# Kernel optimization log

Hardware: AMD Instinct MI355X
Metric: run time of the kernel (lower is better)

## Reference

```python
import jax, jax.numpy as jnp
import numpy as np

N_HEADS = 16
PROJ_DIM = 64  # per-head dim
DIM = N_HEADS * PROJ_DIM  # 1024


def setup_inputs() -> dict:
    key = jax.random.key(0)
    k1, k2, k3, k4, k5 = jax.random.split(key, 5)
    N, L = 2, 2048
    scale = 1.0 / np.sqrt(DIM)
    return {
        "query": jax.random.normal(k1, (N, L, DIM), dtype=jnp.float32),
        "key": jax.random.normal(k2, (N, L, DIM), dtype=jnp.float32),
        "Wq": jax.random.normal(k3, (DIM, DIM), dtype=jnp.float32) * scale,
        "Wk": jax.random.normal(k4, (DIM, DIM), dtype=jnp.float32) * scale,
        "Wv": jax.random.normal(k5, (DIM, DIM), dtype=jnp.float32) * scale,
    }


def reference(query, key, Wq, Wk, Wv):
    # Causal linear-complexity attention (mask=True branch, left_first=False).
    N, Lq, _ = query.shape
    Lk = key.shape[1]
    H, Dh = N_HEADS, PROJ_DIM
    # torch Linear: x @ W.T ; reshape to (N, H, L, Dh)
    q = (query @ Wq.T).reshape(N, Lq, H, Dh).transpose(0, 2, 1, 3)
    k = (key @ Wk.T).reshape(N, Lk, H, Dh).transpose(0, 2, 1, 3)
    v = (key @ Wv.T).reshape(N, Lk, H, Dh).transpose(0, 2, 1, 3)
    q = jax.nn.softmax(q, axis=-1)
    k = jax.nn.softmax(k, axis=-1)
    # right[t] = sum_{s<=t} k_s^T v_s  : (N,H,Lk,Dh,Dh) cumulative outer products
    S = jnp.cumsum(jnp.einsum('nhti,nhtj->nhtij', k, v), axis=2)
    out = jnp.einsum('nhti,nhtij->nhtj', q, S)  # (N,H,Lq,Dh)
    return out.transpose(0, 2, 1, 3).reshape(N, Lq, H * Dh)
```

## Files before the change

### kernel.cpp

```cpp
#include <hip/hip_runtime.h>


constexpr int DIM  = 1024;
constexpr int H    = 16;
constexpr int DH   = 64;
constexpr int LSEQ = 2048;
constexpr int NB   = 2;
constexpr int MTOK = NB * LSEQ;
constexpr int CS   = 64;
constexpr int NC   = LSEQ / CS;

typedef __bf16 bf16x8 __attribute__((ext_vector_type(8)));
typedef float floatx4 __attribute__((ext_vector_type(4)));
typedef unsigned short ushort_t;

__device__ __forceinline__ ushort_t f2bf(float f) {
  unsigned int u = __float_as_uint(f);
  u += 0x7FFFu + ((u >> 16) & 1u);
  return (ushort_t)(u >> 16);
}
__device__ __forceinline__ float bf2f(ushort_t b) {
  return __uint_as_float(((unsigned int)b) << 16);
}

__device__ __forceinline__ void async16(void* lds, const void* g) {
  __builtin_amdgcn_global_load_lds(
      (const __attribute__((address_space(1))) unsigned int*)g,
      (__attribute__((address_space(3))) unsigned int*)lds, 16, 0, 0);
}

__device__ __forceinline__ bf16x8 tfrag(const unsigned int* T, int row, int uoff) {
  union { bf16x8 v; unsigned int u[4]; } r;
  const unsigned int* p = T + row * 33 + uoff;
  r.u[0] = p[0]; r.u[1] = p[1]; r.u[2] = p[2]; r.u[3] = p[3];
  return r.v;
}

__device__ __forceinline__ void transpose_tile(const ushort_t* g, unsigned int* TT, int tid) {
  const int ic = tid & 7, tp = tid >> 3;
  const ushort_t* r0 = g + (size_t)(2 * tp) * DIM + ic * 8;
  union { uint4 q; ushort_t u[8]; } a0, a1;
  a0.q = *(const uint4*)r0;
  a1.q = *(const uint4*)(r0 + DIM);
#pragma unroll
  for (int j = 0; j < 8; j++)
    TT[(8 * ic + j) * 33 + tp] = (unsigned int)a0.u[j] | ((unsigned int)a1.u[j] << 16);
}

__global__ __launch_bounds__(256) void cast_all(const float* __restrict__ q,
                                                const float* __restrict__ k,
                                                const float* __restrict__ wq,
                                                const float* __restrict__ wk,
                                                const float* __restrict__ wv,
                                                ushort_t* __restrict__ xbf,
                                                ushort_t* __restrict__ wbf) {
  const int seg = blockIdx.y;
  const float* src;
  ushort_t* dst;
  int n4;
  if (seg == 0)      { src = q;  dst = xbf;                  n4 = (4 << 20) / 4; }
  else if (seg == 1) { src = k;  dst = xbf + (4 << 20);      n4 = (4 << 20) / 4; }
  else if (seg == 2) { src = wq; dst = wbf;                  n4 = (1 << 20) / 4; }
  else if (seg == 3) { src = wk; dst = wbf + (1 << 20);      n4 = (1 << 20) / 4; }
  else               { src = wv; dst = wbf + (2 << 20);      n4 = (1 << 20) / 4; }
  for (int i = blockIdx.x * 256 + threadIdx.x; i < n4; i += gridDim.x * 256) {
    const float4 f = ((const float4*)src)[i];
    ((ushort4*)dst)[i] = make_ushort4(f2bf(f.x), f2bf(f.y), f2bf(f.z), f2bf(f.w));
  }
}

struct Stage { ushort_t As[128 * 32]; ushort_t Ws[128 * 32]; };
union SMemU { Stage st; ushort_t CsB[128 * 136]; };

__global__ __launch_bounds__(256) void gemm_fused(const ushort_t* __restrict__ xbf,
                                                  const ushort_t* __restrict__ wbf,
                                                  ushort_t* __restrict__ qp,
                                                  ushort_t* __restrict__ kp,
                                                  ushort_t* __restrict__ vp) {
  __shared__ SMemU sm;
  const int tid  = threadIdx.x;
  const int z    = blockIdx.z;
  const ushort_t* A = xbf + (z ? (size_t)(4 << 20) : 0);
  const ushort_t* W = wbf + (size_t)z * (1 << 20);
  ushort_t* C = (z == 0) ? qp : ((z == 1) ? kp : vp);
  const int bn   = blockIdx.x * 128;
  const int bm   = blockIdx.y * 128;
  const int lane = tid & 63;
  const int wid  = tid >> 6;
  const int wm   = wid >> 1, wn = wid & 1;
  const int row16 = lane & 15, quad = lane >> 4;

  floatx4 acc[4][4] = {};

  const ushort_t* gA0 = A + (size_t)(bm + (tid >> 2)) * DIM + (tid & 3) * 8;
  const ushort_t* gA1 = A + (size_t)(bm + 64 + (tid >> 2)) * DIM + (tid & 3) * 8;
  const ushort_t* gW0 = W + (size_t)(bn + (tid >> 2)) * DIM + (tid & 3) * 8;
  const ushort_t* gW1 = W + (size_t)(bn + 64 + (tid >> 2)) * DIM + (tid & 3) * 8;
  ushort_t* lA0 = sm.st.As + tid * 8;
  ushort_t* lA1 = sm.st.As + (tid + 256) * 8;
  ushort_t* lW0 = sm.st.Ws + tid * 8;
  ushort_t* lW1 = sm.st.Ws + (tid + 256) * 8;

  for (int k0 = 0; k0 < DIM; k0 += 32) {
    __syncthreads();
    async16(lA0, gA0 + k0);
    async16(lA1, gA1 + k0);
    async16(lW0, gW0 + k0);
    async16(lW1, gW1 + k0);
    __syncthreads();
    bf16x8 a[4], b[4];
#pragma unroll
    for (int mt = 0; mt < 4; mt++)
      a[mt] = *(const bf16x8*)&sm.st.As[(wm * 64 + mt * 16 + row16) * 32 + quad * 8];
#pragma unroll
    for (int nt = 0; nt < 4; nt++)
      b[nt] = *(const bf16x8*)&sm.st.Ws[(wn * 64 + nt * 16 + row16) * 32 + quad * 8];
#pragma unroll
    for (int mt = 0; mt < 4; mt++)
#pragma unroll
      for (int nt = 0; nt < 4; nt++)
        acc[mt][nt] = __builtin_amdgcn_mfma_f32_16x16x32_bf16(a[mt], b[nt], acc[mt][nt], 0, 0, 0);
  }
  __syncthreads();

  if (z < 2) {
#pragma unroll
    for (int mt = 0; mt < 4; mt++)
#pragma unroll
      for (int r = 0; r < 4; r++) {
        float m = fmaxf(fmaxf(acc[mt][0][r], acc[mt][1][r]),
                        fmaxf(acc[mt][2][r], acc[mt][3][r]));
#pragma unroll
        for (int o = 1; o < 16; o <<= 1) m = fmaxf(m, __shfl_xor(m, o, 64));
        float e[4], s = 0.f;
#pragma unroll
        for (int nt = 0; nt < 4; nt++) { e[nt] = __expf(acc[mt][nt][r] - m); s += e[nt]; }
#pragma unroll
        for (int o = 1; o < 16; o <<= 1) s += __shfl_xor(s, o, 64);
        const float inv = 1.f / s;
#pragma unroll
        for (int nt = 0; nt < 4; nt++) acc[mt][nt][r] = e[nt] * inv;
      }
  }

#pragma unroll
  for (int mt = 0; mt < 4; mt++)
#pragma unroll
    for (int nt = 0; nt < 4; nt++)
#pragma unroll
      for (int r = 0; r < 4; r++)
        sm.CsB[(wm * 64 + mt * 16 + quad * 4 + r) * 136 + wn * 64 + nt * 16 + row16] =
            f2bf(acc[mt][nt][r]);
  __syncthreads();
#pragma unroll
  for (int it = 0; it < 8; it++) {
    const int ch = tid + it * 256;
    const int row = ch >> 4, ic = ch & 15;
    const uint4 val = *(const uint4*)&sm.CsB[row * 136 + ic * 8];
    *(uint4*)&C[(size_t)(bm + row) * DIM + bn + ic * 8] = val;
  }
}

__global__ __launch_bounds__(256) void chunk_T(const ushort_t* __restrict__ kp,
                                               const ushort_t* __restrict__ vp,
                                               float* __restrict__ cs) {
  __shared__ unsigned int KT[64 * 33];
  __shared__ unsigned int VT[64 * 33];
  const int c = blockIdx.x, h = blockIdx.y, n = blockIdx.z;
  const int tid = threadIdx.x;
  const size_t gbase = ((size_t)(n * LSEQ + c * CS)) * DIM + h * DH;

  transpose_tile(kp + gbase, KT, tid);
  transpose_tile(vp + gbase, VT, tid);
  __syncthreads();

  const int lane = tid & 63, wid = tid >> 6;
  const int row16 = lane & 15, quad = lane >> 4;

  floatx4 acc[4] = {};
#pragma unroll
  for (int ks = 0; ks < 2; ks++) {
    const bf16x8 a = tfrag(VT, wid * 16 + row16, ks * 16 + quad * 4);
#pragma unroll
    for (int nt = 0; nt < 4; nt++) {
      const bf16x8 b = tfrag(KT, nt * 16 + row16, ks * 16 + quad * 4);
      acc[nt] = __builtin_amdgcn_mfma_f32_16x16x32_bf16(a, b, acc[nt], 0, 0, 0);
    }
  }
  float* outp = cs + ((size_t)((n * H + h) * NC + c)) * (DH * DH);
#pragma unroll
  for (int nt = 0; nt < 4; nt++)
#pragma unroll
    for (int r = 0; r < 4; r++)
      outp[(wid * 16 + quad * 4 + r) * DH + nt * 16 + row16] = acc[nt][r];
}

__global__ __launch_bounds__(256) void prefix_chunks(const float* __restrict__ cs,
                                                     ushort_t* __restrict__ csb) {
  const int nh = blockIdx.x >> 4;
  const int e  = (blockIdx.x & 15) * 256 + threadIdx.x;
  const float* bf_ = cs + (size_t)nh * NC * (DH * DH) + e;
  ushort_t* bb = csb + (size_t)nh * NC * (DH * DH) + e;
  float run = 0.f;
#pragma unroll
  for (int c = 0; c < NC; c++) {
    const float cur = bf_[(size_t)c * (DH * DH)];
    bb[(size_t)c * (DH * DH)] = f2bf(run);
    run += cur;
  }
}

__global__ __launch_bounds__(256) void attn_mfma(const ushort_t* __restrict__ qp,
                                                 const ushort_t* __restrict__ kp,
                                                 const ushort_t* __restrict__ vp,
                                                 const ushort_t* __restrict__ csb,
                                                 float* __restrict__ out) {
  __shared__ ushort_t Qs[64 * 72];
  __shared__ ushort_t Ks[64 * 72];
  __shared__ ushort_t Ts[64 * 72];
  __shared__ unsigned int VT[64 * 33];
  __shared__ ushort_t Pb[64 * 72];
  const int c = blockIdx.x, h = blockIdx.y, n = blockIdx.z;
  const int tid = threadIdx.x;
  const size_t gbase = ((size_t)(n * LSEQ + c * CS)) * DIM + h * DH;
  const size_t cbase = ((size_t)((n * H + h) * NC + c)) * (DH * DH);

#pragma unroll
  for (int it = 0; it < 2; it++) {
    const int ch = tid + it * 256;
    const int row = ch >> 3, ic = ch & 7;
    *(uint4*)&Qs[row * 72 + ic * 8] = *(const uint4*)&qp[gbase + (size_t)row * DIM + ic * 8];
    *(uint4*)&Ks[row * 72 + ic * 8] = *(const uint4*)&kp[gbase + (size_t)row * DIM + ic * 8];
    *(uint4*)&Ts[row * 72 + ic * 8] = *(const uint4*)&csb[cbase + (size_t)row * DH + ic * 8];
  }
  transpose_tile(vp + gbase, VT, tid);
  __syncthreads();

  const int lane = tid & 63, wid = tid >> 6;
  const int row16 = lane & 15, quad = lane >> 4;
  const int t0 = wid * 16;

  floatx4 acc[4] = {};
  floatx4 pacc[4] = {};

#pragma unroll
  for (int ks = 0; ks < 2; ks++) {
    const bf16x8 aq = *(const bf16x8*)&Qs[(t0 + row16) * 72 + ks * 32 + quad * 8];
#pragma unroll
    for (int nt = 0; nt < 4; nt++) {
      const bf16x8 bt = *(const bf16x8*)&Ts[(nt * 16 + row16) * 72 + ks * 32 + quad * 8];
      acc[nt] = __builtin_amdgcn_mfma_f32_16x16x32_bf16(aq, bt, acc[nt], 0, 0, 0);
      const bf16x8 bk = *(const bf16x8*)&Ks[(nt * 16 + row16) * 72 + ks * 32 + quad * 8];
      pacc[nt] = __builtin_amdgcn_mfma_f32_16x16x32_bf16(aq, bk, pacc[nt], 0, 0, 0);
    }
  }
#pragma unroll
  for (int nt = 0; nt < 4; nt++)
#pragma unroll
    for (int r = 0; r < 4; r++) {
      const int t = t0 + quad * 4 + r, s = nt * 16 + row16;
      Pb[t * 72 + s] = f2bf((s <= t) ? pacc[nt][r] : 0.f);
    }
  __syncthreads();

#pragma unroll
  for (int ks = 0; ks < 2; ks++) {
    const bf16x8 ap = *(const bf16x8*)&Pb[(t0 + row16) * 72 + ks * 32 + quad * 8];
#pragma unroll
    for (int nt = 0; nt < 4; nt++) {
      const bf16x8 bv = tfrag(VT, nt * 16 + row16, ks * 16 + quad * 4);
      acc[nt] = __builtin_amdgcn_mfma_f32_16x16x32_bf16(ap, bv, acc[nt], 0, 0, 0);
    }
  }

#pragma unroll
  for (int nt = 0; nt < 4; nt++)
#pragma unroll
    for (int r = 0; r < 4; r++)
      out[gbase + (size_t)(t0 + quad * 4 + r) * DIM + nt * 16 + row16] = acc[nt][r];
}

extern "C" void kernel_launch(void* const* d_in, const int* in_sizes, int n_in,
                              void* d_out, int out_size, void* d_ws, size_t ws_size,
                              hipStream_t stream) {
  const float* query = (const float*)d_in[0];
  const float* key   = (const float*)d_in[1];
  const float* Wq    = (const float*)d_in[2];
  const float* Wk    = (const float*)d_in[3];
  const float* Wv    = (const float*)d_in[4];
  float* out = (float*)d_out;

  const size_t PM = (size_t)4 << 20;
  ushort_t* qp = (ushort_t*)d_ws;
  ushort_t* kp = qp + PM;
  ushort_t* vp = kp + PM;
  float*    cs = (float*)(vp + PM);
  ushort_t* csb = (ushort_t*)(cs + PM);
  ushort_t* xbf = (ushort_t*)cs;
  ushort_t* wbf = (ushort_t*)out;

  cast_all<<<dim3(512, 5), 256, 0, stream>>>(query, key, Wq, Wk, Wv, xbf, wbf);

  gemm_fused<<<dim3(DIM / 128, MTOK / 128, 3), 256, 0, stream>>>(xbf, wbf, qp, kp, vp);

  chunk_T<<<dim3(NC, H, NB), 256, 0, stream>>>(kp, vp, cs);
  prefix_chunks<<<dim3(NB * H * 16), 256, 0, stream>>>(cs, csb);
  attn_mfma<<<dim3(NC, H, NB), 256, 0, stream>>>(qp, kp, vp, csb, out);
}
```

Baseline: 172.5 us.

## Fuse chunk state and prefix scan, widen GEMM K-step with swizzled LDS

Merges the per-chunk K^T V kernel and the fp32 prefix-sum kernel into one sequential scan kernel per (batch, head). It keeps the running state in registers and writes bf16 exclusive prefixes directly, removing the fp32 intermediate buffer and one launch. The GEMM now loads 64-wide K slices per barrier pair using an XOR-swizzled LDS layout to cut bank conflicts, and uses a flattened 1D grid. The attention kernel reuses the Ts buffer for P to save LDS. The scan runs on only 32 blocks serially over 32 chunks, which risks low parallelism.

```diff
diff --git a/kernel.cpp b/kernel.cpp
--- a/kernel.cpp
+++ b/kernel.cpp
@@ -22,20 +22,17 @@
 __device__ __forceinline__ float bf2f(ushort_t b) {
   return __uint_as_float(((unsigned int)b) << 16);
 }
-
 __device__ __forceinline__ void async16(void* lds, const void* g) {
   __builtin_amdgcn_global_load_lds(
       (const __attribute__((address_space(1))) unsigned int*)g,
       (__attribute__((address_space(3))) unsigned int*)lds, 16, 0, 0);
 }
-
 __device__ __forceinline__ bf16x8 tfrag(const unsigned int* T, int row, int uoff) {
   union { bf16x8 v; unsigned int u[4]; } r;
   const unsigned int* p = T + row * 33 + uoff;
   r.u[0] = p[0]; r.u[1] = p[1]; r.u[2] = p[2]; r.u[3] = p[3];
   return r.v;
 }
-
 __device__ __forceinline__ void transpose_tile(const ushort_t* g, unsigned int* TT, int tid) {
   const int ic = tid & 7, tp = tid >> 3;
   const ushort_t* r0 = g + (size_t)(2 * tp) * DIM + ic * 8;
@@ -69,88 +66,98 @@
   }
 }
 
-struct Stage { ushort_t As[128 * 32]; ushort_t Ws[128 * 32]; };
-union SMemU { Stage st; ushort_t CsB[128 * 136]; };
+union GSm {
+  struct { ushort_t A0[128 * 32]; ushort_t A1[128 * 32];
+           ushort_t W0[128 * 32]; ushort_t W1[128 * 32]; } g;
+  ushort_t CsB[128 * 136];
+};
 
 __global__ __launch_bounds__(256) void gemm_fused(const ushort_t* __restrict__ xbf,
                                                   const ushort_t* __restrict__ wbf,
                                                   ushort_t* __restrict__ qp,
                                                   ushort_t* __restrict__ kp,
                                                   ushort_t* __restrict__ vp) {
-  __shared__ SMemU sm;
-  const int tid  = threadIdx.x;
-  const int z    = blockIdx.z;
+  __shared__ GSm sm;
+  const int tid = threadIdx.x;
+  const int z   = blockIdx.x >> 8;
+  const int r   = blockIdx.x & 255;
+  const int bn  = (r & 7) * 128;
+  const int bm  = (r >> 3) * 128;
   const ushort_t* A = xbf + (z ? (size_t)(4 << 20) : 0);
   const ushort_t* W = wbf + (size_t)z * (1 << 20);
   ushort_t* C = (z == 0) ? qp : ((z == 1) ? kp : vp);
-  const int bn   = blockIdx.x * 128;
-  const int bm   = blockIdx.y * 128;
-  const int lane = tid & 63;
-  const int wid  = tid >> 6;
-  const int wm   = wid >> 1, wn = wid & 1;
+  const int lane = tid & 63, wid = tid >> 6;
+  const int wm = wid >> 1, wn = wid & 1;
   const int row16 = lane & 15, quad = lane >> 4;
 
+  const int row0 = tid >> 2, c0 = tid & 3;
+  const int cg = c0 ^ ((row0 >> 1) & 3);
+  const ushort_t* gA  = A + (size_t)(bm + row0) * DIM + cg * 8;
+  const ushort_t* gA2 = gA + (size_t)64 * DIM;
+  const ushort_t* gW  = W + (size_t)(bn + row0) * DIM + cg * 8;
+  const ushort_t* gW2 = gW + (size_t)64 * DIM;
+
   floatx4 acc[4][4] = {};
-
-  const ushort_t* gA0 = A + (size_t)(bm + (tid >> 2)) * DIM + (tid & 3) * 8;
-  const ushort_t* gA1 = A + (size_t)(bm + 64 + (tid >> 2)) * DIM + (tid & 3) * 8;
-  const ushort_t* gW0 = W + (size_t)(bn + (tid >> 2)) * DIM + (tid & 3) * 8;
-  const ushort_t* gW1 = W + (size_t)(bn + 64 + (tid >> 2)) * DIM + (tid & 3) * 8;
-  ushort_t* lA0 = sm.st.As + tid * 8;
-  ushort_t* lA1 = sm.st.As + (tid + 256) * 8;
-  ushort_t* lW0 = sm.st.Ws + tid * 8;
-  ushort_t* lW1 = sm.st.Ws + (tid + 256) * 8;
-
-  for (int k0 = 0; k0 < DIM; k0 += 32) {
-    __syncthreads();
-    async16(lA0, gA0 + k0);
-    async16(lA1, gA1 + k0);
-    async16(lW0, gW0 + k0);
-    async16(lW1, gW1 + k0);
-    __syncthreads();
-    bf16x8 a[4], b[4];
+  const int cq = quad ^ ((row16 >> 1) & 3);
+
+  for (int k0 = 0; k0 < DIM; k0 += 64) {
+    __syncthreads();
+    async16(sm.g.A0 + tid * 8, gA + k0);
+    async16(sm.g.A0 + (tid + 256) * 8, gA2 + k0);
+    async16(sm.g.A1 + tid * 8, gA + k0 + 32);
+    async16(sm.g.A1 + (tid + 256) * 8, gA2 + k0 + 32);
+    async16(sm.g.W0 + tid * 8, gW + k0);
+    async16(sm.g.W0 + (tid + 256) * 8, gW2 + k0);
+    async16(sm.g.W1 + tid * 8, gW + k0 + 32);
+    async16(sm.g.W1 + (tid + 256) * 8, gW2 + k0 + 32);
+    __syncthreads();
+#pragma unroll
+    for (int ks = 0; ks < 2; ks++) {
+      const ushort_t* As = ks ? sm.g.A1 : sm.g.A0;
+      const ushort_t* Ws = ks ? sm.g.W1 : sm.g.W0;
+      bf16x8 a[4], b[4];
+#pragma unroll
+      for (int mt = 0; mt < 4; mt++)
+        a[mt] = *(const bf16x8*)&As[(wm * 64 + mt * 16 + row16) * 32 + cq * 8];
+#pragma unroll
+      for (int nt = 0; nt < 4; nt++)
+        b[nt] = *(const bf16x8*)&Ws[(wn * 64 + nt * 16 + row16) * 32 + cq * 8];
+#pragma unroll
+      for (int mt = 0; mt < 4; mt++)
+#pragma unroll
+        for (int nt = 0; nt < 4; nt++)
+          acc[mt][nt] = __builtin_amdgcn_mfma_f32_16x16x32_bf16(a[mt], b[nt], acc[mt][nt], 0, 0, 0);
+    }
+  }
+  __syncthreads();
+
+  if (z < 2) {
 #pragma unroll
     for (int mt = 0; mt < 4; mt++)
-      a[mt] = *(const bf16x8*)&sm.st.As[(wm * 64 + mt * 16 + row16) * 32 + quad * 8];
-#pragma unroll
-    for (int nt = 0; nt < 4; nt++)
-      b[nt] = *(const bf16x8*)&sm.st.Ws[(wn * 64 + nt * 16 + row16) * 32 + quad * 8];
-#pragma unroll
-    for (int mt = 0; mt < 4; mt++)
-#pragma unroll
-      for (int nt = 0; nt < 4; nt++)
-        acc[mt][nt] = __builtin_amdgcn_mfma_f32_16x16x32_bf16(a[mt], b[nt], acc[mt][nt], 0, 0, 0);
-  }
-  __syncthreads();
-
-  if (z < 2) {
-#pragma unroll
-    for (int mt = 0; mt < 4; mt++)
-#pragma unroll
-      for (int r = 0; r < 4; r++) {
-        float m = fmaxf(fmaxf(acc[mt][0][r], acc[mt][1][r]),
-                        fmaxf(acc[mt][2][r], acc[mt][3][r]));
+#pragma unroll
+      for (int rr = 0; rr < 4; rr++) {
+        float m = fmaxf(fmaxf(acc[mt][0][rr], acc[mt][1][rr]),
+                        fmaxf(acc[mt][2][rr], acc[mt][3][rr]));
 #pragma unroll
         for (int o = 1; o < 16; o <<= 1) m = fmaxf(m, __shfl_xor(m, o, 64));
         float e[4], s = 0.f;
 #pragma unroll
-        for (int nt = 0; nt < 4; nt++) { e[nt] = __expf(acc[mt][nt][r] - m); s += e[nt]; }
+        for (int nt = 0; nt < 4; nt++) { e[nt] = __expf(acc[mt][nt][rr] - m); s += e[nt]; }
 #pragma unroll
         for (int o = 1; o < 16; o <<= 1) s += __shfl_xor(s, o, 64);
         const float inv = 1.f / s;
 #pragma unroll
-        for (int nt = 0; nt < 4; nt++) acc[mt][nt][r] = e[nt] * inv;
+        for (int nt = 0; nt < 4; nt++) acc[mt][nt][rr] = e[nt] * inv;
       }
   }
-
 #pragma unroll
   for (int mt = 0; mt < 4; mt++)
 #pragma unroll
     for (int nt = 0; nt < 4; nt++)
 #pragma unroll
-      for (int r = 0; r < 4; r++)
-        sm.CsB[(wm * 64 + mt * 16 + quad * 4 + r) * 136 + wn * 64 + nt * 16 + row16] =
-            f2bf(acc[mt][nt][r]);
+      for (int rr = 0; rr < 4; rr++)
+        sm.CsB[(wm * 64 + mt * 16 + quad * 4 + rr) * 136 + wn * 64 + nt * 16 + row16] =
+            f2bf(acc[mt][nt][rr]);
   __syncthreads();
 #pragma unroll
   for (int it = 0; it < 8; it++) {
@@ -161,52 +168,43 @@
   }
 }
 
-__global__ __launch_bounds__(256) void chunk_T(const ushort_t* __restrict__ kp,
-                                               const ushort_t* __restrict__ vp,
-                                               float* __restrict__ cs) {
+__global__ __launch_bounds__(256) void chunk_scan(const ushort_t* __restrict__ kp,
+                                                  const ushort_t* __restrict__ vp,
+                                                  ushort_t* __restrict__ Tpre) {
   __shared__ unsigned int KT[64 * 33];
   __shared__ unsigned int VT[64 * 33];
-  const int c = blockIdx.x, h = blockIdx.y, n = blockIdx.z;
+  const int h = blockIdx.x & 15, n = blockIdx.x >> 4;
   const int tid = threadIdx.x;
-  const size_t gbase = ((size_t)(n * LSEQ + c * CS)) * DIM + h * DH;
-
-  transpose_tile(kp + gbase, KT, tid);
-  transpose_tile(vp + gbase, VT, tid);
-  __syncthreads();
-
   const int lane = tid & 63, wid = tid >> 6;
   const int row16 = lane & 15, quad = lane >> 4;
 
-  floatx4 acc[4] = {};
-#pragma unroll
-  for (int ks = 0; ks < 2; ks++) {
-    const bf16x8 a = tfrag(VT, wid * 16 + row16, ks * 16 + quad * 4);
-#pragma unroll
-    for (int nt = 0; nt < 4; nt++) {
-      const bf16x8 b = tfrag(KT, nt * 16 + row16, ks * 16 + quad * 4);
-      acc[nt] = __builtin_amdgcn_mfma_f32_16x16x32_bf16(a, b, acc[nt], 0, 0, 0);
-    }
-  }
-  float* outp = cs + ((size_t)((n * H + h) * NC + c)) * (DH * DH);
-#pragma unroll
-  for (int nt = 0; nt < 4; nt++)
-#pragma unroll
-    for (int r = 0; r < 4; r++)
-      outp[(wid * 16 + quad * 4 + r) * DH + nt * 16 + row16] = acc[nt][r];
-}
-
-__global__ __launch_bounds__(256) void prefix_chunks(const float* __restrict__ cs,
-                                                     ushort_t* __restrict__ csb) {
-  const int nh = blockIdx.x >> 4;
-  const int e  = (blockIdx.x & 15) * 256 + threadIdx.x;
-  const float* bf_ = cs + (size_t)nh * NC * (DH * DH) + e;
-  ushort_t* bb = csb + (size_t)nh * NC * (DH * DH) + e;
-  float run = 0.f;
-#pragma unroll
+  floatx4 run[4] = {};
   for (int c = 0; c < NC; c++) {
-    const float cur = bf_[(size_t)c * (DH * DH)];
-    bb[(size_t)c * (DH * DH)] = f2bf(run);
-    run += cur;
+    const size_t gbase = ((size_t)(n * LSEQ + c * CS)) * DIM + h * DH;
+    __syncthreads();
+    transpose_tile(kp + gbase, KT, tid);
+    transpose_tile(vp + gbase, VT, tid);
+    __syncthreads();
+
+    ushort_t* outp = Tpre + ((size_t)((n * H + h) * NC + c)) * (DH * DH);
+#pragma unroll
+    for (int nt = 0; nt < 4; nt++)
+#pragma unroll
+      for (int rr = 0; rr < 4; rr++)
+        outp[(wid * 16 + quad * 4 + rr) * DH + nt * 16 + row16] = f2bf(run[nt][rr]);
+
+    floatx4 acc[4] = {};
+#pragma unroll
+    for (int ks = 0; ks < 2; ks++) {
+      const bf16x8 a = tfrag(VT, wid * 16 + row16, ks * 16 + quad * 4);
+#pragma unroll
+      for (int nt = 0; nt < 4; nt++) {
+        const bf16x8 b = tfrag(KT, nt * 16 + row16, ks * 16 + quad * 4);
+        acc[nt] = __builtin_amdgcn_mfma_f32_16x16x32_bf16(a, b, acc[nt], 0, 0, 0);
+      }
+    }
+#pragma unroll
+    for (int nt = 0; nt < 4; nt++) run[nt] += acc[nt];
   }
 }
 
@@ -219,7 +217,6 @@
   __shared__ ushort_t Ks[64 * 72];
   __shared__ ushort_t Ts[64 * 72];
   __shared__ unsigned int VT[64 * 33];
-  __shared__ ushort_t Pb[64 * 72];
   const int c = blockIdx.x, h = blockIdx.y, n = blockIdx.z;
   const int tid = threadIdx.x;
   const size_t gbase = ((size_t)(n * LSEQ + c * CS)) * DIM + h * DH;
@@ -242,7 +239,6 @@
 
   floatx4 acc[4] = {};
   floatx4 pacc[4] = {};
-
 #pragma unroll
   for (int ks = 0; ks < 2; ks++) {
     const bf16x8 aq = *(const bf16x8*)&Qs[(t0 + row16) * 72 + ks * 32 + quad * 8];
@@ -254,30 +250,29 @@
       pacc[nt] = __builtin_amdgcn_mfma_f32_16x16x32_bf16(aq, bk, pacc[nt], 0, 0, 0);
     }
   }
+  __syncthreads();
 #pragma unroll
   for (int nt = 0; nt < 4; nt++)
 #pragma unroll
-    for (int r = 0; r < 4; r++) {
-      const int t = t0 + quad * 4 + r, s = nt * 16 + row16;
-      Pb[t * 72 + s] = f2bf((s <= t) ? pacc[nt][r] : 0.f);
-    }
-  __syncthreads();
-
+    for (int rr = 0; rr < 4; rr++) {
+      const int t = t0 + quad * 4 + rr, s = nt * 16 + row16;
+      Ts[t * 72 + s] = f2bf((s <= t) ? pacc[nt][rr] : 0.f);
+    }
+  __syncthreads();
 #pragma unroll
   for (int ks = 0; ks < 2; ks++) {
-    const bf16x8 ap = *(const bf16x8*)&Pb[(t0 + row16) * 72 + ks * 32 + quad * 8];
+    const bf16x8 ap = *(const bf16x8*)&Ts[(t0 + row16) * 72 + ks * 32 + quad * 8];
 #pragma unroll
     for (int nt = 0; nt < 4; nt++) {
       const bf16x8 bv = tfrag(VT, nt * 16 + row16, ks * 16 + quad * 4);
       acc[nt] = __builtin_amdgcn_mfma_f32_16x16x32_bf16(ap, bv, acc[nt], 0, 0, 0);
     }
   }
-
 #pragma unroll
   for (int nt = 0; nt < 4; nt++)
 #pragma unroll
-    for (int r = 0; r < 4; r++)
-      out[gbase + (size_t)(t0 + quad * 4 + r) * DIM + nt * 16 + row16] = acc[nt][r];
+    for (int rr = 0; rr < 4; rr++)
+      out[gbase + (size_t)(t0 + quad * 4 + rr) * DIM + nt * 16 + row16] = acc[nt][rr];
 }
 
 extern "C" void kernel_launch(void* const* d_in, const int* in_sizes, int n_in,
@@ -290,20 +285,15 @@
   const float* Wv    = (const float*)d_in[4];
   float* out = (float*)d_out;
 
-  const size_t PM = (size_t)4 << 20;
-  ushort_t* qp = (ushort_t*)d_ws;
-  ushort_t* kp = qp + PM;
-  ushort_t* vp = kp + PM;
-  float*    cs = (float*)(vp + PM);
-  ushort_t* csb = (ushort_t*)(cs + PM);
-  ushort_t* xbf = (ushort_t*)cs;
-  ushort_t* wbf = (ushort_t*)out;
+  ushort_t* qp   = (ushort_t*)d_ws;
+  ushort_t* kp   = qp + (4 << 20);
+  ushort_t* vp   = kp + (4 << 20);
+  ushort_t* Tpre = vp + (4 << 20);
+  ushort_t* xbf  = Tpre;
+  ushort_t* wbf  = (ushort_t*)out;
 
   cast_all<<<dim3(512, 5), 256, 0, stream>>>(query, key, Wq, Wk, Wv, xbf, wbf);
-
-  gemm_fused<<<dim3(DIM / 128, MTOK / 128, 3), 256, 0, stream>>>(xbf, wbf, qp, kp, vp);
-
-  chunk_T<<<dim3(NC, H, NB), 256, 0, stream>>>(kp, vp, cs);
-  prefix_chunks<<<dim3(NB * H * 16), 256, 0, stream>>>(cs, csb);
-  attn_mfma<<<dim3(NC, H, NB), 256, 0, stream>>>(qp, kp, vp, csb, out);
-}
+  gemm_fused<<<dim3(768), 256, 0, stream>>>(xbf, wbf, qp, kp, vp);
+  chunk_scan<<<dim3(NB * H), 256, 0, stream>>>(kp, vp, Tpre);
+  attn_mfma<<<dim3(NC, H, NB), 256, 0, stream>>>(qp, kp, vp, Tpre, out);
+}
```

After: 177.7 us. +3.0%, slower.
